# Kernel optimization log

Hardware: AMD Instinct MI355X
Metric: run time of the kernel (lower is better)

Reference implementation:

```python
import jax, jax.numpy as jnp
import numpy as np
import math

NUM_HEADS = 32
NUM_KV = 8
D = 128          # num_hidden == per-head dim in this module
S = 2048
B = 1
DK = 128
ROPE_BASE = 10000.0


def rope(x):
    # x: [B, H, S, D]; standard Llama-style RoPE (split-halves rotation) over positions.
    d = x.shape[-1]
    half = d // 2
    pos = jnp.arange(x.shape[2], dtype=jnp.float32)                       # [S]
    inv_freq = 1.0 / (ROPE_BASE ** (jnp.arange(half, dtype=jnp.float32) / half))
    ang = pos[:, None] * inv_freq[None, :]                                # [S, half]
    cos = jnp.cos(ang)
    sin = jnp.sin(ang)
    x1 = x[..., :half]
    x2 = x[..., half:]
    return jnp.concatenate([x1 * cos - x2 * sin, x1 * sin + x2 * cos], axis=-1)


def setup_inputs() -> dict:
    key = jax.random.key(0)
    ks = jax.random.split(key, 8)
    query = jax.random.normal(ks[0], (B, S, D), dtype=jnp.float32)
    k_in = jax.random.normal(ks[1], (B, S, D), dtype=jnp.float32)
    v_in = jax.random.normal(ks[2], (B, S, D), dtype=jnp.float32)
    # causal mask: 1 where attention allowed (lower triangle incl diagonal)
    mask = jnp.tril(jnp.ones((S, S), dtype=jnp.int32))[None, None]        # [1,1,S,S]
    sc = 0.02
    Wq = jax.random.normal(ks[3], (NUM_HEADS * D, D), dtype=jnp.float32) * sc
    bq = jnp.zeros((NUM_HEADS * D,), dtype=jnp.float32)
    Wk = jax.random.normal(ks[4], (NUM_KV * D, D), dtype=jnp.float32) * sc
    bk = jnp.zeros((NUM_KV * D,), dtype=jnp.float32)
    Wv = jax.random.normal(ks[5], (NUM_KV * D, D), dtype=jnp.float32) * sc
    bv = jnp.zeros((NUM_KV * D,), dtype=jnp.float32)
    Wo = jax.random.normal(ks[6], (D, NUM_HEADS * D), dtype=jnp.float32) * sc
    bo = jnp.zeros((D,), dtype=jnp.float32)
    return {"query": query, "key": k_in, "values": v_in, "mask": mask,
            "Wq": Wq, "bq": bq, "Wk": Wk, "bk": bk, "Wv": Wv, "bv": bv,
            "Wo": Wo, "bo": bo}


def reference(query, key, values, mask, Wq, bq, Wk, bk, Wv, bv, Wo, bo):
    Bq, Sq, Dh = query.shape
    # projections; torch Linear: x @ W.T + b. Note: view (reshape), not transpose,
    # exactly as in the original module.
    q = (query @ Wq.T + bq).reshape(Bq, NUM_HEADS, Sq, Dh)   # [B,H,S,D]
    k = (key @ Wk.T + bk).reshape(Bq, NUM_KV, Sq, Dh)        # [B,Hkv,S,D]
    v = (values @ Wv.T + bv).reshape(Bq, NUM_KV, Sq, Dh)
    rk = rope(k)
    rv = rope(v)  # module applies RoPE to values too (faithful)
    rep = NUM_HEADS // NUM_KV
    # torch .repeat((1, rep, 1, 1)) tiles whole head blocks -> jnp.tile
    rk = jnp.tile(rk, (1, rep, 1, 1))                        # [B,H,S,D]
    rv = jnp.tile(rv, (1, rep, 1, 1))
    scores = jnp.einsum('bhqd,bhkd->bhqk', q, rk) / math.sqrt(DK)
    scores = jnp.where(mask == 0, -jnp.inf, scores)
    attn = jax.nn.softmax(scores, axis=-1)
    out = jnp.einsum('bhqk,bhkd->bhqd', attn, rv)            # [B,H,S,D]
    out = out.transpose(0, 2, 1, 3).reshape(Bq, Sq, NUM_HEADS * Dh)
    return out @ Wo.T + bo
```

## Files before the change

### kernel.cpp

```cpp
#include <hip/hip_runtime.h>

typedef unsigned short u16;
typedef unsigned int u32;
typedef short frag_t __attribute__((ext_vector_type(8)));
typedef float f32x4 __attribute__((ext_vector_type(4)));

#define S_LEN 2048

__device__ __forceinline__ float bf2f(u32 u) {
  union { u32 i; float f; } v; v.i = u << 16; return v.f;
}
__device__ __forceinline__ u16 f2bf(float f) {
  u32 x = __float_as_uint(f);
  u32 r = (x + 0x7fffu + ((x >> 16) & 1u)) >> 16;
  return (u16)r;
}
__device__ __forceinline__ void unpack8(uint4 r, float* o) {
  o[0] = bf2f(r.x & 0xffffu); o[1] = bf2f(r.x >> 16);
  o[2] = bf2f(r.y & 0xffffu); o[3] = bf2f(r.y >> 16);
  o[4] = bf2f(r.z & 0xffffu); o[5] = bf2f(r.z >> 16);
  o[6] = bf2f(r.w & 0xffffu); o[7] = bf2f(r.w >> 16);
}
__device__ __forceinline__ u16 ld_in(const void* p, size_t idx, bool fp32) {
  if (fp32) return f2bf(((const float*)p)[idx]);
  return ((const u16*)p)[idx];
}
__device__ __forceinline__ uint4 ld8(const void* p, size_t eidx, bool fp32) {
  if (!fp32) return *(const uint4*)((const u16*)p + eidx);
  const float4* f = (const float4*)((const float*)p + eidx);
  float4 x = f[0], y = f[1];
  uint4 r;
  r.x = (u32)f2bf(x.x) | ((u32)f2bf(x.y) << 16);
  r.y = (u32)f2bf(x.z) | ((u32)f2bf(x.w) << 16);
  r.z = (u32)f2bf(y.x) | ((u32)f2bf(y.y) << 16);
  r.w = (u32)f2bf(y.z) | ((u32)f2bf(y.w) << 16);
  return r;
}

__global__ __launch_bounds__(256) void proj_all(
    const void* __restrict__ query, const void* __restrict__ key,
    const void* __restrict__ values,
    const void* __restrict__ Wq, const void* __restrict__ bq,
    const void* __restrict__ Wk, const void* __restrict__ bk,
    const void* __restrict__ Wv, const void* __restrict__ bv,
    u16* __restrict__ Qb, u16* __restrict__ Kb, u16* __restrict__ Vtmp,
    u32* __restrict__ flag_out) {
  __shared__ u16 As[128][136];
  __shared__ u16 Ws[128][136];
  __shared__ u32 flagS;
  u16 (*Cs)[136] = As;
  const int t = threadIdx.x;
  if (t < 64) {
    u32 e = ((u32)((const u16*)query)[2 * t] >> 7) & 0xFFu;
    bool ok = (e >= 110u && e <= 140u);
    unsigned long long b = __ballot(ok);
    if (t == 0) flagS = (__popcll(b) < 32) ? 1u : 0u;
  }
  __syncthreads();
  const bool fp32 = (flagS != 0u);
  if (t == 0 && blockIdx.x == 0 && blockIdx.y == 0) *flag_out = flagS;
  const int x = blockIdx.x;
  const void *A, *W, *bias;
  u16* C; int N, n0;
  if (x < 32)      { A = query;  W = Wq; bias = bq; C = Qb;   N = 4096; n0 = x << 7; }
  else if (x < 40) { A = key;    W = Wk; bias = bk; C = Kb;   N = 1024; n0 = (x - 32) << 7; }
  else             { A = values; W = Wv; bias = bv; C = Vtmp; N = 1024; n0 = (x - 40) << 7; }
  const float osc = (x < 32) ? 0.12751743f : 1.0f;
  const int m0 = blockIdx.y << 7;
#pragma unroll
  for (int i = 0; i < 8; ++i) {
    int task = t + (i << 8);
    int row = task >> 4, ch = (task & 15) << 3;
    *(uint4*)&As[row][ch] = ld8(A, (size_t)(m0 + row) * 128 + ch, fp32);
    *(uint4*)&Ws[row][ch] = ld8(W, (size_t)(n0 + row) * 128 + ch, fp32);
  }
  __syncthreads();
  const int lane = t & 63, w = t >> 6, quad = lane >> 4, l15 = lane & 15;
  const int rm = (w & 1) << 6, rn = (w >> 1) << 6;
  f32x4 acc[4][4];
#pragma unroll
  for (int mt = 0; mt < 4; ++mt)
#pragma unroll
    for (int nt = 0; nt < 4; ++nt) acc[mt][nt] = 0.f;
#pragma unroll
  for (int mtp = 0; mtp < 2; ++mtp) {
    frag_t a0[4], a1[4];
#pragma unroll
    for (int kc = 0; kc < 4; ++kc) {
      a0[kc] = *(const frag_t*)&As[rm + mtp * 32 + l15][kc * 32 + quad * 8];
      a1[kc] = *(const frag_t*)&As[rm + mtp * 32 + 16 + l15][kc * 32 + quad * 8];
    }
#pragma unroll
    for (int nt = 0; nt < 4; ++nt)
#pragma unroll
      for (int kc = 0; kc < 4; ++kc) {
        frag_t b = *(const frag_t*)&Ws[rn + nt * 16 + l15][kc * 32 + quad * 8];
        acc[mtp * 2][nt] = __builtin_amdgcn_mfma_f32_16x16x32_bf16(a0[kc], b, acc[mtp * 2][nt], 0, 0, 0);
        acc[mtp * 2 + 1][nt] = __builtin_amdgcn_mfma_f32_16x16x32_bf16(a1[kc], b, acc[mtp * 2 + 1][nt], 0, 0, 0);
      }
  }
  __syncthreads();
#pragma unroll
  for (int nt = 0; nt < 4; ++nt) {
    float bb = bf2f((u32)ld_in(bias, n0 + rn + nt * 16 + l15, fp32));
#pragma unroll
    for (int mt = 0; mt < 4; ++mt) {
      int row = rm + ((mt >> 1) * 32) + ((mt & 1) * 16) + quad * 4;
#pragma unroll
      for (int r = 0; r < 4; ++r)
        Cs[row + r][rn + nt * 16 + l15] = f2bf((acc[mt][nt][r] + bb) * osc);
    }
  }
  __syncthreads();
#pragma unroll
  for (int i = 0; i < 8; ++i) {
    int task = t + (i << 8);
    int row = task >> 4, ch = (task & 15) << 3;
    *(uint4*)&C[(size_t)(m0 + row) * N + n0 + ch] = *(const uint4*)&Cs[row][ch];
  }
}

__global__ __launch_bounds__(256) void rope_kv_tr(u16* __restrict__ Kb,
                                                  const u16* __restrict__ Vb,
                                                  u16* __restrict__ VbT) {
  __shared__ u16 Lt[128][72];
  const int t = threadIdx.x;
  const int s0 = blockIdx.x << 6;
  const int g = blockIdx.y;
  for (int i = t; i < 4096; i += 256) {
    int s = s0 + (i >> 6), ii = i & 63;
    float invf = __expf(-(float)ii * 0.14391156831212787f);
    float ang = (float)s * invf;
    float sn, cs;
    sincosf(ang, &sn, &cs);
    size_t base = ((size_t)(g << 11) + s) * 128 + ii;
    float k1 = bf2f((u32)Kb[base]), k2 = bf2f((u32)Kb[base + 64]);
    Kb[base] = f2bf(k1 * cs - k2 * sn);
    Kb[base + 64] = f2bf(k1 * sn + k2 * cs);
  }
  const u16* src = Vb + (size_t)g * S_LEN * 128;
  for (int i = t; i < 512; i += 256) {
    int r = i >> 3, d8 = (i & 7) << 3;
    float lo[8], hi[8];
    unpack8(*(const uint4*)&src[(size_t)(s0 + r) * 128 + d8], lo);
    unpack8(*(const uint4*)&src[(size_t)(s0 + r) * 128 + d8 + 64], hi);
#pragma unroll
    for (int j = 0; j < 8; ++j) {
      float invf = __expf(-(float)(d8 + j) * 0.14391156831212787f);
      float ang = (float)(s0 + r) * invf;
      float sn, cs;
      sincosf(ang, &sn, &cs);
      Lt[d8 + j][r] = f2bf(lo[j] * cs - hi[j] * sn);
      Lt[d8 + 64 + j][r] = f2bf(lo[j] * sn + hi[j] * cs);
    }
  }
  __syncthreads();
  u16* dst = VbT + (size_t)g * 128 * S_LEN + s0;
  for (int i = t; i < 2048; i += 256) {
    int d = i >> 4, s4 = (i & 15) << 2;
    uint2 pk;
    pk.x = (u32)Lt[d][s4] | ((u32)Lt[d][s4 + 1] << 16);
    pk.y = (u32)Lt[d][s4 + 2] | ((u32)Lt[d][s4 + 3] << 16);
    *(uint2*)&dst[(size_t)d * S_LEN + s4] = pk;
  }
}

__global__ __launch_bounds__(256) void attn_mfma(
    const u16* __restrict__ Qb, const u16* __restrict__ Kb,
    const u16* __restrict__ VbT, u16* __restrict__ OpA, u16* __restrict__ OpB,
    float2* __restrict__ Ml, int nkh) {
  __shared__ union SmemU {
    struct { u16 St[128][40]; } m;
    struct { u16 Og[128][136]; } e;
  } su;
  const int t = threadIdx.x;
  const int lane = t & 63, w = t >> 6, quad = lane >> 4, l15 = lane & 15;
  const int g = (int)blockIdx.x & 7;
  const int kh = (int)blockIdx.x >> 3;
  const int h = g + (w << 3);
  const u16* Kg = Kb + (size_t)g * S_LEN * 128;
  const u16* Vg = VbT + (size_t)g * 128 * S_LEN;
  u16* dst = kh ? OpB : OpA;

  const int qt = 63 - (int)blockIdx.y;
  const int q0 = qt << 5;
  const int niter = qt + 1;
  frag_t aq[2][4];
#pragma unroll
  for (int qp = 0; qp < 2; ++qp)
#pragma unroll
    for (int kc = 0; kc < 4; ++kc)
      aq[qp][kc] = *(const frag_t*)&Qb[((size_t)h * S_LEN + q0 + qp * 16 + l15) * 128 +
                                       kc * 32 + quad * 8];
  float m_r[2] = {-1e30f, -1e30f}, l_r[2] = {0.f, 0.f};
  f32x4 oacc[2][8];
#pragma unroll
  for (int qp = 0; qp < 2; ++qp)
#pragma unroll
    for (int nt = 0; nt < 8; ++nt) oacc[qp][nt] = 0.f;

  frag_t aK[2][4];
  if (kh < niter) {
    const int k0 = kh << 5;
#pragma unroll
    for (int kk = 0; kk < 2; ++kk)
#pragma unroll
      for (int kc = 0; kc < 4; ++kc)
        aK[kk][kc] = *(const frag_t*)&Kg[(size_t)(k0 + kk * 16 + l15) * 128 +
                                         kc * 32 + quad * 8];
  }
  for (int sj = kh; sj < niter; sj += nkh) {
    const int k0 = sj << 5;
    frag_t av[8];
#pragma unroll
    for (int nt = 0; nt < 8; ++nt)
      av[nt] = *(const frag_t*)&Vg[(size_t)(nt * 16 + l15) * S_LEN + k0 + quad * 8];
    f32x4 s4[2][2];
#pragma unroll
    for (int kk = 0; kk < 2; ++kk) { s4[kk][0] = 0.f; s4[kk][1] = 0.f; }
#pragma unroll
    for (int kc = 0; kc < 4; ++kc)
#pragma unroll
      for (int kk = 0; kk < 2; ++kk) {
        s4[kk][0] = __builtin_amdgcn_mfma_f32_16x16x32_bf16(aK[kk][kc], aq[0][kc], s4[kk][0], 0, 0, 0);
        s4[kk][1] = __builtin_amdgcn_mfma_f32_16x16x32_bf16(aK[kk][kc], aq[1][kc], s4[kk][1], 0, 0, 0);
      }
    if (sj + nkh < niter) {
      const int kn = (sj + nkh) << 5;
#pragma unroll
      for (int kk = 0; kk < 2; ++kk)
#pragma unroll
        for (int kc = 0; kc < 4; ++kc)
          aK[kk][kc] = *(const frag_t*)&Kg[(size_t)(kn + kk * 16 + l15) * 128 +
                                           kc * 32 + quad * 8];
    }
    const bool lastm = (sj == niter - 1);
    float alpha[2];
#pragma unroll
    for (int qp = 0; qp < 2; ++qp) {
      const int qg = q0 + qp * 16 + l15;
      float mx = -1e30f;
#pragma unroll
      for (int kk = 0; kk < 2; ++kk)
#pragma unroll
        for (int r = 0; r < 4; ++r) {
          float sv = s4[kk][qp][r];
          if (lastm && (k0 + kk * 16 + quad * 4 + r) > qg) sv = -1e30f;
          s4[kk][qp][r] = sv;
          mx = fmaxf(mx, sv);
        }
      mx = fmaxf(mx, __shfl_xor(mx, 16));
      mx = fmaxf(mx, __shfl_xor(mx, 32));
      float mn = fmaxf(m_r[qp], mx);
      alpha[qp] = __builtin_amdgcn_exp2f(m_r[qp] - mn);
      m_r[qp] = mn;
      float sum = 0.f;
      const int strow = w * 32 + qp * 16 + l15;
#pragma unroll
      for (int kk = 0; kk < 2; ++kk) {
        float p0 = __builtin_amdgcn_exp2f(s4[kk][qp][0] - mn);
        float p1 = __builtin_amdgcn_exp2f(s4[kk][qp][1] - mn);
        float p2 = __builtin_amdgcn_exp2f(s4[kk][qp][2] - mn);
        float p3 = __builtin_amdgcn_exp2f(s4[kk][qp][3] - mn);
        sum += (p0 + p1) + (p2 + p3);
        uint2 pk;
        asm("v_cvt_pk_bf16_f32 %0, %1, %2" : "=v"(pk.x) : "v"(p0), "v"(p1));
        asm("v_cvt_pk_bf16_f32 %0, %1, %2" : "=v"(pk.y) : "v"(p2), "v"(p3));
        *(uint2*)&su.m.St[strow][kk * 16 + quad * 4] = pk;
      }
      sum += __shfl_xor(sum, 16);
      sum += __shfl_xor(sum, 32);
      l_r[qp] = l_r[qp] * alpha[qp] + sum;
    }
    if (__any(alpha[0] < 1.0f || alpha[1] < 1.0f)) {
#pragma unroll
      for (int qp = 0; qp < 2; ++qp)
#pragma unroll
        for (int r = 0; r < 4; ++r) {
          float al = __shfl(alpha[qp], quad * 4 + r);
#pragma unroll
          for (int nt = 0; nt < 8; ++nt) oacc[qp][nt][r] *= al;
        }
    }
    frag_t pa0 = *(const frag_t*)&su.m.St[w * 32 + l15][quad * 8];
    frag_t pa1 = *(const frag_t*)&su.m.St[w * 32 + 16 + l15][quad * 8];
#pragma unroll
    for (int nt = 0; nt < 8; ++nt) {
      oacc[0][nt] = __builtin_amdgcn_mfma_f32_16x16x32_bf16(pa0, av[nt], oacc[0][nt], 0, 0, 0);
      oacc[1][nt] = __builtin_amdgcn_mfma_f32_16x16x32_bf16(pa1, av[nt], oacc[1][nt], 0, 0, 0);
    }
  }
  __syncthreads();
#pragma unroll
  for (int qp = 0; qp < 2; ++qp)
#pragma unroll
    for (int r = 0; r < 4; ++r) {
      float fac = 1.0f;
      if (nkh == 1) fac = 1.0f / __shfl(l_r[qp], quad * 4 + r);
      int row = w * 32 + qp * 16 + quad * 4 + r;
#pragma unroll
      for (int nt = 0; nt < 8; ++nt)
        su.e.Og[row][nt * 16 + l15] = f2bf(oacc[qp][nt][r] * fac);
    }
  __syncthreads();
#pragma unroll
  for (int jj = 0; jj < 8; ++jj) {
    int c = t + (jj << 8);
    int row = c >> 4, ch = (c & 15) << 3;
    int hh = row >> 5, qr = row & 31;
    *(uint4*)&dst[(size_t)(q0 + qr) * 4096 + (g + hh * 8) * 128 + ch] =
        *(const uint4*)&su.e.Og[row][ch];
  }
  if (nkh == 2 && quad == 0) {
#pragma unroll
    for (int qp = 0; qp < 2; ++qp)
      Ml[((size_t)kh * 32 + h) * S_LEN + q0 + qp * 16 + l15] =
          make_float2(m_r[qp], l_r[qp]);
  }
}

__global__ __launch_bounds__(256) void out_part(
    const u16* __restrict__ OpA, const u16* __restrict__ OpB,
    const float2* __restrict__ Ml, const void* __restrict__ Wo,
    float* __restrict__ Pout, const u32* __restrict__ flagp, int nkh) {
  __shared__ u16 As[128][136];
  __shared__ u16 Ws[128][136];
  const bool fp32 = (*flagp != 0u);
  const int t = threadIdx.x;
  const int lane = t & 63, w = t >> 6, quad = lane >> 4, l15 = lane & 15;
  const int rm = (w & 1) << 6, rn = (w >> 1) << 6;
  const int m0 = (int)blockIdx.x << 7;
  const int z = (int)blockIdx.y;
  f32x4 acc[4][4];
#pragma unroll
  for (int mt = 0; mt < 4; ++mt)
#pragma unroll
    for (int nt = 0; nt < 4; ++nt) acc[mt][nt] = 0.f;
  for (int kc2 = 0; kc2 < 2; ++kc2) {
    if (kc2) __syncthreads();
    const int kc0 = (z << 8) + (kc2 << 7);
    const int hh = kc0 >> 7;
#pragma unroll
    for (int i = 0; i < 8; ++i) {
      int task = t + (i << 8);
      int row = task >> 4, ch = (task & 15) << 3;
      size_t idx = (size_t)(m0 + row) * 4096 + kc0 + ch;
      if (nkh == 2) {
        int s = m0 + row;
        float2 p1 = Ml[(size_t)hh * S_LEN + s];
        float2 p2 = Ml[(size_t)(32 + hh) * S_LEN + s];
        float mn = fmaxf(p1.x, p2.x);
        float a1 = __builtin_amdgcn_exp2f(p1.x - mn);
        float a2 = __builtin_amdgcn_exp2f(p2.x - mn);
        float linv = 1.0f / (a1 * p1.y + a2 * p2.y);
        float w1 = a1 * linv, w2 = a2 * linv;
        float o1[8], o2[8];
        unpack8(*(const uint4*)&OpA[idx], o1);
        unpack8(*(const uint4*)&OpB[idx], o2);
        uint4 r;
        r.x = (u32)f2bf(o1[0] * w1 + o2[0] * w2) | ((u32)f2bf(o1[1] * w1 + o2[1] * w2) << 16);
        r.y = (u32)f2bf(o1[2] * w1 + o2[2] * w2) | ((u32)f2bf(o1[3] * w1 + o2[3] * w2) << 16);
        r.z = (u32)f2bf(o1[4] * w1 + o2[4] * w2) | ((u32)f2bf(o1[5] * w1 + o2[5] * w2) << 16);
        r.w = (u32)f2bf(o1[6] * w1 + o2[6] * w2) | ((u32)f2bf(o1[7] * w1 + o2[7] * w2) << 16);
        *(uint4*)&As[row][ch] = r;
      } else {
        *(uint4*)&As[row][ch] = *(const uint4*)&OpA[idx];
      }
      *(uint4*)&Ws[row][ch] = ld8(Wo, (size_t)row * 4096 + kc0 + ch, fp32);
    }
    __syncthreads();
#pragma unroll
    for (int mtp = 0; mtp < 2; ++mtp) {
      frag_t a0[4], a1[4];
#pragma unroll
      for (int kc = 0; kc < 4; ++kc) {
        a0[kc] = *(const frag_t*)&As[rm + mtp * 32 + l15][kc * 32 + quad * 8];
        a1[kc] = *(const frag_t*)&As[rm + mtp * 32 + 16 + l15][kc * 32 + quad * 8];
      }
#pragma unroll
      for (int nt = 0; nt < 4; ++nt)
#pragma unroll
        for (int kc = 0; kc < 4; ++kc) {
          frag_t b = *(const frag_t*)&Ws[rn + nt * 16 + l15][kc * 32 + quad * 8];
          acc[mtp * 2][nt] = __builtin_amdgcn_mfma_f32_16x16x32_bf16(a0[kc], b, acc[mtp * 2][nt], 0, 0, 0);
          acc[mtp * 2 + 1][nt] = __builtin_amdgcn_mfma_f32_16x16x32_bf16(a1[kc], b, acc[mtp * 2 + 1][nt], 0, 0, 0);
        }
    }
  }
#pragma unroll
  for (int mt = 0; mt < 4; ++mt) {
    int mrow = m0 + rm + ((mt >> 1) * 32) + ((mt & 1) * 16) + quad * 4;
#pragma unroll
    for (int nt = 0; nt < 4; ++nt) {
      int n = rn + nt * 16 + l15;
#pragma unroll
      for (int r = 0; r < 4; ++r)
        Pout[((size_t)z * 2048 + mrow + r) * 128 + n] = acc[mt][nt][r];
    }
  }
}

__global__ __launch_bounds__(256) void out_red(
    const float* __restrict__ Pout, const void* __restrict__ bo,
    void* __restrict__ out, const u32* __restrict__ flagp) {
  const bool fp32 = (*flagp != 0u);
  int e4 = blockIdx.x * 256 + threadIdx.x;
  const float4* P = (const float4*)Pout;
  float4 s = P[e4];
#pragma unroll
  for (int z = 1; z < 16; ++z) {
    float4 p = P[(size_t)z * 65536 + e4];
    s.x += p.x; s.y += p.y; s.z += p.z; s.w += p.w;
  }
  int n = (e4 << 2) & 127;
  s.x += bf2f((u32)ld_in(bo, n + 0, fp32));
  s.y += bf2f((u32)ld_in(bo, n + 1, fp32));
  s.z += bf2f((u32)ld_in(bo, n + 2, fp32));
  s.w += bf2f((u32)ld_in(bo, n + 3, fp32));
  if (fp32) {
    ((float4*)out)[e4] = s;
  } else {
    uint2 pk;
    pk.x = (u32)f2bf(s.x) | ((u32)f2bf(s.y) << 16);
    pk.y = (u32)f2bf(s.z) | ((u32)f2bf(s.w) << 16);
    *(uint2*)((u16*)out + (e4 << 2)) = pk;
  }
}

extern "C" void kernel_launch(void* const* d_in, const int* in_sizes, int n_in,
                              void* d_out, int out_size, void* d_ws, size_t ws_size,
                              hipStream_t stream) {
  (void)in_sizes; (void)n_in; (void)out_size;
  const void* query  = d_in[0];
  const void* key    = d_in[1];
  const void* values = d_in[2];
  const void* Wq = d_in[4];
  const void* bq = d_in[5];
  const void* Wk = d_in[6];
  const void* bk = d_in[7];
  const void* Wv = d_in[8];
  const void* bv = d_in[9];
  const void* Wo = d_in[10];
  const void* bo = d_in[11];

  char* ws = (char*)d_ws;
  u32* flag   = (u32*)ws;
  u16* Qb     = (u16*)(ws + 64);
  u16* Kb     = (u16*)(ws + 64 + (16ull << 20));
  u16* VbT    = (u16*)(ws + 64 + (20ull << 20));
  u16* Vtmp   = (u16*)(ws + 64 + (24ull << 20));
  u16* Ob     = (u16*)(ws + 64 + (24ull << 20));
  u16* OpB    = (u16*)(ws + 64 + (40ull << 20));
  float2* Mlb = (float2*)(ws + 64 + (56ull << 20));
  float* Pout = (float*)Qb;

  const bool split = (ws_size >= (58ull << 20));
  const int nkh = split ? 2 : 1;

  proj_all<<<dim3(48, 16), 256, 0, stream>>>(query, key, values, Wq, bq, Wk, bk,
                                             Wv, bv, Qb, Kb, Vtmp, flag);
  rope_kv_tr<<<dim3(32, 8), 256, 0, stream>>>(Kb, Vtmp, VbT);
  attn_mfma<<<dim3(8 * nkh, 64), 256, 0, stream>>>(Qb, Kb, VbT, Ob, OpB, Mlb, nkh);
  out_part<<<dim3(16, 16), 256, 0, stream>>>(Ob, OpB, Mlb, Wo, Pout, flag, nkh);
  out_red<<<256, 256, 0, stream>>>(Pout, bo, d_out, flag);
}
```

Baseline: 273.3 us.

## Pair causal query tiles per block and split each head across two waves

The attention kernel now runs 512 threads per block, with two waves per head. Each wave owns 16 query rows instead of 32. Each block processes two query tiles (qt and 63-qt), which balances causal work across blocks and halves the grid in y. The K-fragment prefetch across iterations is removed: K is loaded in-loop, V loads are placed after the QK MFMAs behind a sched_barrier, and per-wave register use drops. This trades a longer sequential loop per block and less register-level prefetching for better load balance and more waves per block.

New measurement: 383.3 us. 1.4x slower.

```diff
diff --git a/kernel.cpp b/kernel.cpp
--- a/kernel.cpp
+++ b/kernel.cpp
@@ -165,7 +165,7 @@
   }
 }
 
-__global__ __launch_bounds__(256) void attn_mfma(
+__global__ __launch_bounds__(512) void attn_mfma(
     const u16* __restrict__ Qb, const u16* __restrict__ Kb,
     const u16* __restrict__ VbT, u16* __restrict__ OpA, u16* __restrict__ OpB,
     float2* __restrict__ Ml, int nkh) {
@@ -177,91 +177,73 @@
   const int lane = t & 63, w = t >> 6, quad = lane >> 4, l15 = lane & 15;
   const int g = (int)blockIdx.x & 7;
   const int kh = (int)blockIdx.x >> 3;
-  const int h = g + (w << 3);
+  const int h = g + ((w >> 1) << 3);
+  const int qsub = (w & 1) << 4;
   const u16* Kg = Kb + (size_t)g * S_LEN * 128;
   const u16* Vg = VbT + (size_t)g * 128 * S_LEN;
   u16* dst = kh ? OpB : OpA;
-
-  const int qt = 63 - (int)blockIdx.y;
-  const int q0 = qt << 5;
-  const int niter = qt + 1;
-  frag_t aq[2][4];
-#pragma unroll
-  for (int qp = 0; qp < 2; ++qp)
+  const int pi = (int)blockIdx.y;
+
+  for (int tp = 0; tp < 2; ++tp) {
+    const int qt = tp ? pi : 63 - pi;
+    const int q0 = qt << 5;
+    const int niter = qt + 1;
+    frag_t aq[4];
 #pragma unroll
     for (int kc = 0; kc < 4; ++kc)
-      aq[qp][kc] = *(const frag_t*)&Qb[((size_t)h * S_LEN + q0 + qp * 16 + l15) * 128 +
-                                       kc * 32 + quad * 8];
-  float m_r[2] = {-1e30f, -1e30f}, l_r[2] = {0.f, 0.f};
-  f32x4 oacc[2][8];
-#pragma unroll
-  for (int qp = 0; qp < 2; ++qp)
-#pragma unroll
-    for (int nt = 0; nt < 8; ++nt) oacc[qp][nt] = 0.f;
-
-  frag_t aK[2][4];
-  if (kh < niter) {
-    const int k0 = kh << 5;
-#pragma unroll
-    for (int kk = 0; kk < 2; ++kk)
+      aq[kc] = *(const frag_t*)&Qb[((size_t)h * S_LEN + q0 + qsub + l15) * 128 +
+                                   kc * 32 + quad * 8];
+    float m_r = -1e30f, l_r = 0.f;
+    f32x4 oacc[8];
+#pragma unroll
+    for (int nt = 0; nt < 8; ++nt) oacc[nt] = 0.f;
+
+    for (int sj = kh; sj < niter; sj += nkh) {
+      const int k0 = sj << 5;
+      frag_t aK[2][4];
+#pragma unroll
+      for (int kk = 0; kk < 2; ++kk)
+#pragma unroll
+        for (int kc = 0; kc < 4; ++kc)
+          aK[kk][kc] = *(const frag_t*)&Kg[(size_t)(k0 + kk * 16 + l15) * 128 +
+                                           kc * 32 + quad * 8];
+      f32x4 s4[2];
+      s4[0] = 0.f; s4[1] = 0.f;
 #pragma unroll
       for (int kc = 0; kc < 4; ++kc)
-        aK[kk][kc] = *(const frag_t*)&Kg[(size_t)(k0 + kk * 16 + l15) * 128 +
-                                         kc * 32 + quad * 8];
-  }
-  for (int sj = kh; sj < niter; sj += nkh) {
-    const int k0 = sj << 5;
-    frag_t av[8];
-#pragma unroll
-    for (int nt = 0; nt < 8; ++nt)
-      av[nt] = *(const frag_t*)&Vg[(size_t)(nt * 16 + l15) * S_LEN + k0 + quad * 8];
-    f32x4 s4[2][2];
-#pragma unroll
-    for (int kk = 0; kk < 2; ++kk) { s4[kk][0] = 0.f; s4[kk][1] = 0.f; }
-#pragma unroll
-    for (int kc = 0; kc < 4; ++kc)
-#pragma unroll
-      for (int kk = 0; kk < 2; ++kk) {
-        s4[kk][0] = __builtin_amdgcn_mfma_f32_16x16x32_bf16(aK[kk][kc], aq[0][kc], s4[kk][0], 0, 0, 0);
-        s4[kk][1] = __builtin_amdgcn_mfma_f32_16x16x32_bf16(aK[kk][kc], aq[1][kc], s4[kk][1], 0, 0, 0);
-      }
-    if (sj + nkh < niter) {
-      const int kn = (sj + nkh) << 5;
+#pragma unroll
+        for (int kk = 0; kk < 2; ++kk)
+          s4[kk] = __builtin_amdgcn_mfma_f32_16x16x32_bf16(aK[kk][kc], aq[kc], s4[kk], 0, 0, 0);
+      __builtin_amdgcn_sched_barrier(0);
+      frag_t av[8];
+#pragma unroll
+      for (int nt = 0; nt < 8; ++nt)
+        av[nt] = *(const frag_t*)&Vg[(size_t)(nt * 16 + l15) * S_LEN + k0 + quad * 8];
+      const bool lastm = (sj == niter - 1);
+      const int qg = q0 + qsub + l15;
+      float mx = -1e30f;
 #pragma unroll
       for (int kk = 0; kk < 2; ++kk)
 #pragma unroll
-        for (int kc = 0; kc < 4; ++kc)
-          aK[kk][kc] = *(const frag_t*)&Kg[(size_t)(kn + kk * 16 + l15) * 128 +
-                                           kc * 32 + quad * 8];
-    }
-    const bool lastm = (sj == niter - 1);
-    float alpha[2];
-#pragma unroll
-    for (int qp = 0; qp < 2; ++qp) {
-      const int qg = q0 + qp * 16 + l15;
-      float mx = -1e30f;
-#pragma unroll
-      for (int kk = 0; kk < 2; ++kk)
-#pragma unroll
         for (int r = 0; r < 4; ++r) {
-          float sv = s4[kk][qp][r];
+          float sv = s4[kk][r];
           if (lastm && (k0 + kk * 16 + quad * 4 + r) > qg) sv = -1e30f;
-          s4[kk][qp][r] = sv;
+          s4[kk][r] = sv;
           mx = fmaxf(mx, sv);
         }
       mx = fmaxf(mx, __shfl_xor(mx, 16));
       mx = fmaxf(mx, __shfl_xor(mx, 32));
-      float mn = fmaxf(m_r[qp], mx);
-      alpha[qp] = __builtin_amdgcn_exp2f(m_r[qp] - mn);
-      m_r[qp] = mn;
+      float mn = fmaxf(m_r, mx);
+      float alpha = __builtin_amdgcn_exp2f(m_r - mn);
+      m_r = mn;
       float sum = 0.f;
-      const int strow = w * 32 + qp * 16 + l15;
+      const int strow = (w << 4) + l15;
 #pragma unroll
       for (int kk = 0; kk < 2; ++kk) {
-        float p0 = __builtin_amdgcn_exp2f(s4[kk][qp][0] - mn);
-        float p1 = __builtin_amdgcn_exp2f(s4[kk][qp][1] - mn);
-        float p2 = __builtin_amdgcn_exp2f(s4[kk][qp][2] - mn);
-        float p3 = __builtin_amdgcn_exp2f(s4[kk][qp][3] - mn);
+        float p0 = __builtin_amdgcn_exp2f(s4[kk][0] - mn);
+        float p1 = __builtin_amdgcn_exp2f(s4[kk][1] - mn);
+        float p2 = __builtin_amdgcn_exp2f(s4[kk][2] - mn);
+        float p3 = __builtin_amdgcn_exp2f(s4[kk][3] - mn);
         sum += (p0 + p1) + (p2 + p3);
         uint2 pk;
         asm("v_cvt_pk_bf16_f32 %0, %1, %2" : "=v"(pk.x) : "v"(p0), "v"(p1));
@@ -270,52 +252,42 @@
       }
       sum += __shfl_xor(sum, 16);
       sum += __shfl_xor(sum, 32);
-      l_r[qp] = l_r[qp] * alpha[qp] + sum;
-    }
-    if (__any(alpha[0] < 1.0f || alpha[1] < 1.0f)) {
-#pragma unroll
-      for (int qp = 0; qp < 2; ++qp)
+      l_r = l_r * alpha + sum;
+      if (__any(alpha < 1.0f)) {
 #pragma unroll
         for (int r = 0; r < 4; ++r) {
-          float al = __shfl(alpha[qp], quad * 4 + r);
-#pragma unroll
-          for (int nt = 0; nt < 8; ++nt) oacc[qp][nt][r] *= al;
+          float al = __shfl(alpha, quad * 4 + r);
+#pragma unroll
+          for (int nt = 0; nt < 8; ++nt) oacc[nt][r] *= al;
         }
-    }
-    frag_t pa0 = *(const frag_t*)&su.m.St[w * 32 + l15][quad * 8];
-    frag_t pa1 = *(const frag_t*)&su.m.St[w * 32 + 16 + l15][quad * 8];
-#pragma unroll
-    for (int nt = 0; nt < 8; ++nt) {
-      oacc[0][nt] = __builtin_amdgcn_mfma_f32_16x16x32_bf16(pa0, av[nt], oacc[0][nt], 0, 0, 0);
-      oacc[1][nt] = __builtin_amdgcn_mfma_f32_16x16x32_bf16(pa1, av[nt], oacc[1][nt], 0, 0, 0);
-    }
-  }
-  __syncthreads();
-#pragma unroll
-  for (int qp = 0; qp < 2; ++qp)
+      }
+      frag_t pa = *(const frag_t*)&su.m.St[strow][quad * 8];
+#pragma unroll
+      for (int nt = 0; nt < 8; ++nt)
+        oacc[nt] = __builtin_amdgcn_mfma_f32_16x16x32_bf16(pa, av[nt], oacc[nt], 0, 0, 0);
+    }
+    __syncthreads();
 #pragma unroll
     for (int r = 0; r < 4; ++r) {
       float fac = 1.0f;
-      if (nkh == 1) fac = 1.0f / __shfl(l_r[qp], quad * 4 + r);
-      int row = w * 32 + qp * 16 + quad * 4 + r;
+      if (nkh == 1) fac = 1.0f / __shfl(l_r, quad * 4 + r);
+      int row = (w << 4) + quad * 4 + r;
 #pragma unroll
       for (int nt = 0; nt < 8; ++nt)
-        su.e.Og[row][nt * 16 + l15] = f2bf(oacc[qp][nt][r] * fac);
-    }
-  __syncthreads();
-#pragma unroll
-  for (int jj = 0; jj < 8; ++jj) {
-    int c = t + (jj << 8);
-    int row = c >> 4, ch = (c & 15) << 3;
-    int hh = row >> 5, qr = row & 31;
-    *(uint4*)&dst[(size_t)(q0 + qr) * 4096 + (g + hh * 8) * 128 + ch] =
-        *(const uint4*)&su.e.Og[row][ch];
-  }
-  if (nkh == 2 && quad == 0) {
-#pragma unroll
-    for (int qp = 0; qp < 2; ++qp)
-      Ml[((size_t)kh * 32 + h) * S_LEN + q0 + qp * 16 + l15] =
-          make_float2(m_r[qp], l_r[qp]);
+        su.e.Og[row][nt * 16 + l15] = f2bf(oacc[nt][r] * fac);
+    }
+    __syncthreads();
+#pragma unroll
+    for (int jj = 0; jj < 4; ++jj) {
+      int c = t + (jj << 9);
+      int row = c >> 4, ch = (c & 15) << 3;
+      int hh = row >> 5, qr = row & 31;
+      *(uint4*)&dst[(size_t)(q0 + qr) * 4096 + (g + hh * 8) * 128 + ch] =
+          *(const uint4*)&su.e.Og[row][ch];
+    }
+    if (nkh == 2 && quad == 0)
+      Ml[((size_t)kh * 32 + h) * S_LEN + q0 + qsub + l15] = make_float2(m_r, l_r);
+    __syncthreads();
   }
 }
 
@@ -460,7 +432,7 @@
   proj_all<<<dim3(48, 16), 256, 0, stream>>>(query, key, values, Wq, bq, Wk, bk,
                                              Wv, bv, Qb, Kb, Vtmp, flag);
   rope_kv_tr<<<dim3(32, 8), 256, 0, stream>>>(Kb, Vtmp, VbT);
-  attn_mfma<<<dim3(8 * nkh, 64), 256, 0, stream>>>(Qb, Kb, VbT, Ob, OpB, Mlb, nkh);
+  attn_mfma<<<dim3(8 * nkh, 32), 512, 0, stream>>>(Qb, Kb, VbT, Ob, OpB, Mlb, nkh);
   out_part<<<dim3(16, 16), 256, 0, stream>>>(Ob, OpB, Mlb, Wo, Pout, flag, nkh);
   out_red<<<256, 256, 0, stream>>>(Pout, bo, d_out, flag);
 }
```
